# Optimization experiments

Measured on AMD Instinct MI355X. Metric: run time of the kernel, lower is better.

Reference implementation:

```python
import jax, jax.numpy as jnp
import numpy as np

B, S, HID = 2, 2048, 4096
H, HKV = 32, 8
D = HID // H  # 128
THETA = 10000.0


def rope(x, positions):
    # x: [B, S, h, D]; rotate-half RoPE
    half = D // 2
    inv_freq = 1.0 / (THETA ** (jnp.arange(0, half, dtype=jnp.float32) / half))
    ang = positions[:, None].astype(jnp.float32) * inv_freq[None, :]  # [S, half]
    cos = jnp.cos(ang)[None, :, None, :]
    sin = jnp.sin(ang)[None, :, None, :]
    x1, x2 = x[..., :half], x[..., half:]
    return jnp.concatenate([x1 * cos - x2 * sin, x2 * cos + x1 * sin], axis=-1)


def setup_inputs() -> dict:
    key = jax.random.key(0)
    k1, k2, k3, k4, k5 = jax.random.split(key, 5)
    sc = 1.0 / np.sqrt(HID)
    return {
        "x": jax.random.normal(k1, (B, S, HID), dtype=jnp.float32),
        "wq": jax.random.normal(k2, (HID, HID), dtype=jnp.float32) * sc,
        "wk": jax.random.normal(k3, (HID, HKV * D), dtype=jnp.float32) * sc,
        "wv": jax.random.normal(k4, (HID, HKV * D), dtype=jnp.float32) * sc,
        "wo": jax.random.normal(k5, (HID, HID), dtype=jnp.float32) * sc,
    }


def reference(x, wq, wk, wv, wo):
    pos = jnp.arange(S)
    q = (x @ wq).reshape(B, S, H, D)
    k = (x @ wk).reshape(B, S, HKV, D)
    v = (x @ wv).reshape(B, S, HKV, D)
    q = rope(q, pos)
    k = rope(k, pos)
    # GQA: repeat kv heads to match query heads
    rep = H // HKV
    k = jnp.repeat(k, rep, axis=2)  # [B, S, H, D]
    v = jnp.repeat(v, rep, axis=2)
    scale = 1.0 / jnp.sqrt(jnp.float32(D))
    scores = jnp.einsum('bqhd,bkhd->bhqk', q, k) * scale  # [B, H, S, S]
    causal = jnp.tril(jnp.ones((S, S), dtype=bool))
    scores = jnp.where(causal[None, None], scores, jnp.finfo(scores.dtype).min)
    attn = jax.nn.softmax(scores, axis=-1)
    out = jnp.einsum('bhqk,bkhd->bqhd', attn, v).reshape(B, S, HID)
    return out @ wo
```

## Files before the change

kernel.cpp:

```cpp
#include <hip/hip_runtime.h>

#define BATCH 2
#define SEQ   2048
#define HIDSZ 4096
#define NH    32
#define NKV   8
#define HD    128
#define HALFD 64
#define MROWS (BATCH*SEQ)
#define KVDIM (NKV*HD)

typedef _Float16 f16;
typedef __attribute__((ext_vector_type(4))) float    fx4;
typedef __attribute__((ext_vector_type(4))) _Float16 half4;
typedef __attribute__((ext_vector_type(8))) _Float16 half8;

__device__ __forceinline__ float ldf(const f16* p)   { return (float)*p; }
__device__ __forceinline__ float ldf(const float* p) { return *p; }
__device__ __forceinline__ void  stf(f16* p, float v)   { *p = (f16)v; }
__device__ __forceinline__ void  stf(float* p, float v) { *p = v; }

template<typename T> struct avec;
template<> struct avec<float> { using type = fx4; };
template<> struct avec<f16>   { using type = half4; };

__device__ __forceinline__ half4 toh4(fx4 v) {
    half4 h; h[0] = (f16)v[0]; h[1] = (f16)v[1]; h[2] = (f16)v[2]; h[3] = (f16)v[3];
    return h;
}
__device__ __forceinline__ half4 toh4(half4 v) { return v; }

template<typename TA, typename TC>
__global__ __launch_bounds__(256)
void gemm_mfma(const TA* __restrict__ A, const float* __restrict__ B,
               TC* __restrict__ C, int M, int N, int K) {
    __shared__ f16 As[128][32];
    __shared__ f16 Bs[128][32];
    const int tid  = threadIdx.x;
    const int wave = tid >> 6, lane = tid & 63;
    const int c    = lane & 15, qd = lane >> 4;
    const int wr   = (wave >> 1) * 64, wc = (wave & 1) * 64;
    const int bx = blockIdx.x, by = blockIdx.y;

    const int am = tid >> 3;
    const int ak = (tid & 7) * 4;
    const int bn = (tid & 31) * 4;
    const int bk = (tid >> 5) * 4;

    const TA*    Ap = A + (size_t)(by * 128 + am) * K + ak;
    const float* Bp = B + (size_t)bk * N + bx * 128 + bn;

    fx4 acc[4][4];
#pragma unroll
    for (int i = 0; i < 4; i++)
#pragma unroll
        for (int j = 0; j < 4; j++)
#pragma unroll
            for (int r = 0; r < 4; r++) acc[i][j][r] = 0.f;

    using AT = typename avec<TA>::type;
    AT  areg[4];
    fx4 breg[4];
#pragma unroll
    for (int u = 0; u < 4; u++) {
        areg[u] = *(const AT*)(Ap + (size_t)u * 32 * K);
        breg[u] = *(const fx4*)(Bp + (size_t)u * N);
    }

    for (int k0 = 0; k0 < K; k0 += 32) {
#pragma unroll
        for (int u = 0; u < 4; u++)
            *(half4*)&As[am + u * 32][ak] = toh4(areg[u]);
#pragma unroll
        for (int v = 0; v < 4; v++) {
            const int n  = bn + v;
            const int kx = bk ^ (8 * ((n >> 2) & 3));
            half4 h;
#pragma unroll
            for (int u = 0; u < 4; u++) h[u] = (f16)breg[u][v];
            *(half4*)&Bs[n][kx] = h;
        }
        __syncthreads();
        if (k0 + 32 < K) {
#pragma unroll
            for (int u = 0; u < 4; u++) {
                areg[u] = *(const AT*)(Ap + (size_t)u * 32 * K + (k0 + 32));
                breg[u] = *(const fx4*)(Bp + (size_t)(k0 + 32 + u) * N);
            }
        }
        half8 af[4], bf[4];
#pragma unroll
        for (int i = 0; i < 4; i++)
            af[i] = *(const half8*)&As[wr + i * 16 + c][qd * 8];
#pragma unroll
        for (int j = 0; j < 4; j++) {
            const int n = wc + j * 16 + c;
            bf[j] = *(const half8*)&Bs[n][(qd * 8) ^ (8 * ((n >> 2) & 3))];
        }
#pragma unroll
        for (int i = 0; i < 4; i++)
#pragma unroll
            for (int j = 0; j < 4; j++)
                acc[i][j] = __builtin_amdgcn_mfma_f32_16x16x32_f16(
                                af[i], bf[j], acc[i][j], 0, 0, 0);
        __syncthreads();
    }

#pragma unroll
    for (int i = 0; i < 4; i++)
#pragma unroll
        for (int j = 0; j < 4; j++)
#pragma unroll
            for (int r = 0; r < 4; r++)
                stf(&C[(size_t)(by * 128 + wr + i * 16 + qd * 4 + r) * N
                       + bx * 128 + wc + j * 16 + c], acc[i][j][r]);
}

template<typename T>
__global__ void rope_kernel(T* __restrict__ t, int heads) {
    int idx = blockIdx.x * blockDim.x + threadIdx.x;
    int i   = idx & (HALFD - 1);
    int r   = idx >> 6;
    int h   = r % heads;
    int row = r / heads;
    int pos = row & (SEQ - 1);
    float inv_freq = expf(-(float)i * (9.210340371976184f / 64.0f));
    float ang = (float)pos * inv_freq;
    float s, c;
    sincosf(ang, &s, &c);
    size_t base = (size_t)row * ((size_t)heads * HD) + (size_t)h * HD;
    float x1 = ldf(&t[base + i]);
    float x2 = ldf(&t[base + i + HALFD]);
    stf(&t[base + i],         x1 * c - x2 * s);
    stf(&t[base + i + HALFD], x2 * c + x1 * s);
}

__global__ __launch_bounds__(256)
void transpose_v_kernel(const f16* __restrict__ v, f16* __restrict__ vt) {
    __shared__ short tile[32][33];
    int ts = blockIdx.x * 32;
    int td = blockIdx.y * 32;
    int bk = blockIdx.z;
    int b = bk >> 3, kvh = bk & 7;
    int tx = threadIdx.x & 31, ty = threadIdx.x >> 5;
    const short* vp = (const short*)v;
    short* vtp = (short*)vt;
#pragma unroll
    for (int i = 0; i < 4; i++) {
        int s = ts + ty + i * 8;
        tile[ty + i * 8][tx] = vp[(size_t)(b * SEQ + s) * KVDIM + kvh * HD + td + tx];
    }
    __syncthreads();
#pragma unroll
    for (int i = 0; i < 4; i++) {
        int d = td + ty + i * 8;
        vtp[((size_t)(b * NKV + kvh) * HD + d) * SEQ + ts + tx] = tile[tx][ty + i * 8];
    }
}

__global__ __launch_bounds__(256)
void flash_attn_kernel(const f16* __restrict__ q, const f16* __restrict__ k,
                       const f16* __restrict__ vt, f16* __restrict__ ao) {
    const int NT = SEQ / 64;
    int h = blockIdx.y, b = blockIdx.z;
    int kvh = h >> 2;
    int tid = threadIdx.x;
    int wave = tid >> 6, lane = tid & 63;
    int col = lane & 15, quad = lane >> 4;

    __shared__ f16 Ks[64 * 128];
    __shared__ f16 Vs[128 * 64];
    __shared__ f16 Ps[4 * 16 * 64];

    const f16* kg0 = k  + (size_t)(b * SEQ) * KVDIM + kvh * HD;
    const f16* vg0 = vt + ((size_t)(b * NKV + kvh) * HD) * SEQ;
    const float scale = 0.08838834764831845f;

#pragma unroll 1
    for (int hf = 0; hf < 2; ++hf) {
        const int qv  = hf ? (NT - 1 - (int)blockIdx.x) : (int)blockIdx.x;
        const int q0  = qv * 64;
        const int nkv = qv + 1;

        half8 qf[4];
        {
            const f16* qbase = q +
                (size_t)(b * SEQ + q0 + wave * 16 + col) * HIDSZ + h * HD + quad * 8;
#pragma unroll
            for (int ks = 0; ks < 4; ks++)
                qf[ks] = *(const half8*)(qbase + ks * 32);
        }

        float m_i[4], l_i[4];
#pragma unroll
        for (int r = 0; r < 4; r++) { m_i[r] = -1e30f; l_i[r] = 0.f; }
        fx4 O[8];
#pragma unroll
        for (int n = 0; n < 8; n++)
#pragma unroll
            for (int r = 0; r < 4; r++) O[n][r] = 0.f;

        half8 kreg[4], vreg[4];
#pragma unroll
        for (int i = 0; i < 4; i++) {
            int c2 = tid + i * 256, row = c2 >> 4, d0 = (c2 & 15) * 8;
            kreg[i] = *(const half8*)(kg0 + (size_t)row * KVDIM + d0);
        }
#pragma unroll
        for (int i = 0; i < 4; i++) {
            int c2 = tid + i * 256, row = c2 >> 3, s0 = (c2 & 7) * 8;
            vreg[i] = *(const half8*)(vg0 + (size_t)row * SEQ + s0);
        }
        __syncthreads();
#pragma unroll
        for (int i = 0; i < 4; i++) {
            int c2 = tid + i * 256, row = c2 >> 4, d0 = (c2 & 15) * 8;
            *(half8*)&Ks[row * 128 + (d0 ^ ((row & 7) << 3))] = kreg[i];
        }
#pragma unroll
        for (int i = 0; i < 4; i++) {
            int c2 = tid + i * 256, row = c2 >> 3, s0 = (c2 & 7) * 8;
            *(half8*)&Vs[row * 64 + (s0 ^ ((row & 7) << 3))] = vreg[i];
        }
        __syncthreads();

#pragma unroll 1
        for (int t = 0; t < nkv; ++t) {
            const int j0  = t * 64;
            const bool pre = (t + 1 < nkv);
            if (pre) {
                const int jn = j0 + 64;
#pragma unroll
                for (int i = 0; i < 4; i++) {
                    int c2 = tid + i * 256, row = c2 >> 4, d0 = (c2 & 15) * 8;
                    kreg[i] = *(const half8*)(kg0 + (size_t)(jn + row) * KVDIM + d0);
                }
#pragma unroll
                for (int i = 0; i < 4; i++) {
                    int c2 = tid + i * 256, row = c2 >> 3, s0 = (c2 & 7) * 8;
                    vreg[i] = *(const half8*)(vg0 + (size_t)row * SEQ + jn + s0);
                }
            }
            fx4 S[4];
#pragma unroll
            for (int nt = 0; nt < 4; nt++) {
                fx4 acc;
#pragma unroll
                for (int r = 0; r < 4; r++) acc[r] = 0.f;
                const int row = nt * 16 + col;
#pragma unroll
                for (int ks = 0; ks < 4; ks++) {
                    half8 kf = *(const half8*)&Ks[row * 128 +
                                   ((ks * 32 + quad * 8) ^ ((row & 7) << 3))];
                    acc = __builtin_amdgcn_mfma_f32_16x16x32_f16(qf[ks], kf, acc, 0, 0, 0);
                }
#pragma unroll
                for (int r = 0; r < 4; r++) S[nt][r] = acc[r] * scale;
            }
            if (j0 == q0) {
                int rowb = wave * 16 + quad * 4;
#pragma unroll
                for (int nt = 0; nt < 4; nt++)
#pragma unroll
                    for (int r = 0; r < 4; r++)
                        if (nt * 16 + col > rowb + r) S[nt][r] = -1e30f;
            }
            float mn[4], alpha[4];
#pragma unroll
            for (int r = 0; r < 4; r++) {
                float mx = fmaxf(fmaxf(S[0][r], S[1][r]), fmaxf(S[2][r], S[3][r]));
#pragma unroll
                for (int d = 8; d >= 1; d >>= 1) mx = fmaxf(mx, __shfl_xor(mx, d, 64));
                mn[r] = fmaxf(m_i[r], mx);
                alpha[r] = __expf(m_i[r] - mn[r]);
                m_i[r] = mn[r];
            }
#pragma unroll
            for (int nt = 0; nt < 4; nt++)
#pragma unroll
                for (int r = 0; r < 4; r++) S[nt][r] = __expf(S[nt][r] - mn[r]);
#pragma unroll
            for (int r = 0; r < 4; r++) {
                float s = (S[0][r] + S[1][r]) + (S[2][r] + S[3][r]);
#pragma unroll
                for (int d = 8; d >= 1; d >>= 1) s += __shfl_xor(s, d, 64);
                l_i[r] = l_i[r] * alpha[r] + s;
            }
#pragma unroll
            for (int n = 0; n < 8; n++)
#pragma unroll
                for (int r = 0; r < 4; r++) O[n][r] *= alpha[r];
#pragma unroll
            for (int nt = 0; nt < 4; nt++)
#pragma unroll
                for (int r = 0; r < 4; r++) {
                    int prow = quad * 4 + r;
                    Ps[wave * 1024 + prow * 64 +
                       ((nt * 16 + col) ^ ((prow & 7) << 3))] = (f16)S[nt][r];
                }
            half8 pf[2];
#pragma unroll
            for (int ks2 = 0; ks2 < 2; ks2++)
                pf[ks2] = *(const half8*)&Ps[wave * 1024 + col * 64 +
                              ((ks2 * 32 + quad * 8) ^ ((col & 7) << 3))];
#pragma unroll
            for (int n = 0; n < 8; n++) {
                const int row = n * 16 + col;
#pragma unroll
                for (int ks2 = 0; ks2 < 2; ks2++) {
                    half8 vf = *(const half8*)&Vs[row * 64 +
                                   ((ks2 * 32 + quad * 8) ^ ((row & 7) << 3))];
                    O[n] = __builtin_amdgcn_mfma_f32_16x16x32_f16(pf[ks2], vf, O[n], 0, 0, 0);
                }
            }
            if (pre) {
                __syncthreads();
#pragma unroll
                for (int i = 0; i < 4; i++) {
                    int c2 = tid + i * 256, row = c2 >> 4, d0 = (c2 & 15) * 8;
                    *(half8*)&Ks[row * 128 + (d0 ^ ((row & 7) << 3))] = kreg[i];
                }
#pragma unroll
                for (int i = 0; i < 4; i++) {
                    int c2 = tid + i * 256, row = c2 >> 3, s0 = (c2 & 7) * 8;
                    *(half8*)&Vs[row * 64 + (s0 ^ ((row & 7) << 3))] = vreg[i];
                }
                __syncthreads();
            }
        }

#pragma unroll
        for (int r = 0; r < 4; r++) l_i[r] = 1.f / l_i[r];
        int orow = q0 + wave * 16 + quad * 4;
#pragma unroll
        for (int n = 0; n < 8; n++)
#pragma unroll
            for (int r = 0; r < 4; r++)
                ao[(size_t)(b * SEQ + orow + r) * HIDSZ + h * HD + n * 16 + col] =
                    (f16)(O[n][r] * l_i[r]);
    }
}

extern "C" void kernel_launch(void* const* d_in, const int* in_sizes, int n_in,
                              void* d_out, int out_size, void* d_ws, size_t ws_size,
                              hipStream_t stream) {
    const float* x  = (const float*)d_in[0];
    const float* wq = (const float*)d_in[1];
    const float* wk = (const float*)d_in[2];
    const float* wv = (const float*)d_in[3];
    const float* wo = (const float*)d_in[4];
    float* out = (float*)d_out;

    f16* q  = (f16*)d_ws;
    f16* k  = q + (size_t)MROWS * HIDSZ;
    f16* v  = k + (size_t)MROWS * KVDIM;
    f16* ao = v + (size_t)MROWS * KVDIM;
    f16* vt = ao + (size_t)MROWS * HIDSZ;

    gemm_mfma<float, f16><<<dim3(HIDSZ / 128, MROWS / 128), 256, 0, stream>>>(
        x, wq, q, MROWS, HIDSZ, HIDSZ);
    gemm_mfma<float, f16><<<dim3(KVDIM / 128, MROWS / 128), 256, 0, stream>>>(
        x, wk, k, MROWS, KVDIM, HIDSZ);
    gemm_mfma<float, f16><<<dim3(KVDIM / 128, MROWS / 128), 256, 0, stream>>>(
        x, wv, v, MROWS, KVDIM, HIDSZ);

    rope_kernel<f16><<<(MROWS * NH * HALFD) / 256, 256, 0, stream>>>(q, NH);
    rope_kernel<f16><<<(MROWS * NKV * HALFD) / 256, 256, 0, stream>>>(k, NKV);

    transpose_v_kernel<<<dim3(SEQ / 32, HD / 32, BATCH * NKV), 256, 0, stream>>>(v, vt);

    flash_attn_kernel<<<dim3(SEQ / 128, NH, BATCH), 256, 0, stream>>>(q, k, vt, ao);

    gemm_mfma<f16, float><<<dim3(HIDSZ / 128, MROWS / 128), 256, 0, stream>>>(
        ao, wo, out, MROWS, HIDSZ, HIDSZ);
}
```

Before: 1.159 ms.

## Pad GEMM LDS tiles, remap B loads to scalar columns, swizzle block order

Pads the As/Bs shared tiles from 32 to 40 halves per row, which replaces the XOR swizzle as the way to avoid LDS bank conflicts. The B tile load is remapped so each thread reads scalar floats along four k rows for strided columns, instead of float4 vectors along n, and writes one contiguous half4 per column. Workgroup IDs are remapped in groups of 8 to change the tile visiting order for L2 reuse. The cost is narrower global loads for B (four scalar loads instead of one vector load per row) and more LDS footprint.

```diff
diff --git a/kernel.cpp b/kernel.cpp
--- a/kernel.cpp
+++ b/kernel.cpp
@@ -34,21 +34,25 @@
 __global__ __launch_bounds__(256)
 void gemm_mfma(const TA* __restrict__ A, const float* __restrict__ B,
                TC* __restrict__ C, int M, int N, int K) {
-    __shared__ f16 As[128][32];
-    __shared__ f16 Bs[128][32];
+    __shared__ f16 As[128][40];
+    __shared__ f16 Bs[128][40];
     const int tid  = threadIdx.x;
     const int wave = tid >> 6, lane = tid & 63;
     const int c    = lane & 15, qd = lane >> 4;
     const int wr   = (wave >> 1) * 64, wc = (wave & 1) * 64;
-    const int bx = blockIdx.x, by = blockIdx.y;
+
+    const int nwg = gridDim.x * gridDim.y;
+    const int lin = blockIdx.y * gridDim.x + blockIdx.x;
+    const int swz = (lin & 7) * (nwg >> 3) + (lin >> 3);
+    const int bx  = swz % gridDim.x, by = swz / gridDim.x;
 
     const int am = tid >> 3;
     const int ak = (tid & 7) * 4;
-    const int bn = (tid & 31) * 4;
-    const int bk = (tid >> 5) * 4;
+    const int bc = tid & 31;
+    const int kb = (tid >> 5) * 4;
 
     const TA*    Ap = A + (size_t)(by * 128 + am) * K + ak;
-    const float* Bp = B + (size_t)bk * N + bx * 128 + bn;
+    const float* Bp = B + (size_t)kb * N + bx * 128 + bc;
 
     fx4 acc[4][4];
 #pragma unroll
@@ -59,12 +63,14 @@
             for (int r = 0; r < 4; r++) acc[i][j][r] = 0.f;
 
     using AT = typename avec<TA>::type;
-    AT  areg[4];
-    fx4 breg[4];
+    AT    areg[4];
+    float breg[4][4];
 #pragma unroll
     for (int u = 0; u < 4; u++) {
         areg[u] = *(const AT*)(Ap + (size_t)u * 32 * K);
-        breg[u] = *(const fx4*)(Bp + (size_t)u * N);
+#pragma unroll
+        for (int kk = 0; kk < 4; kk++)
+            breg[u][kk] = Bp[(size_t)kk * N + u * 32];
     }
 
     for (int k0 = 0; k0 < K; k0 += 32) {
@@ -72,20 +78,20 @@
         for (int u = 0; u < 4; u++)
             *(half4*)&As[am + u * 32][ak] = toh4(areg[u]);
 #pragma unroll
-        for (int v = 0; v < 4; v++) {
-            const int n  = bn + v;
-            const int kx = bk ^ (8 * ((n >> 2) & 3));
+        for (int u = 0; u < 4; u++) {
             half4 h;
 #pragma unroll
-            for (int u = 0; u < 4; u++) h[u] = (f16)breg[u][v];
-            *(half4*)&Bs[n][kx] = h;
+            for (int kk = 0; kk < 4; kk++) h[kk] = (f16)breg[u][kk];
+            *(half4*)&Bs[bc + u * 32][kb] = h;
         }
         __syncthreads();
         if (k0 + 32 < K) {
 #pragma unroll
             for (int u = 0; u < 4; u++) {
                 areg[u] = *(const AT*)(Ap + (size_t)u * 32 * K + (k0 + 32));
-                breg[u] = *(const fx4*)(Bp + (size_t)(k0 + 32 + u) * N);
+#pragma unroll
+                for (int kk = 0; kk < 4; kk++)
+                    breg[u][kk] = Bp[(size_t)(k0 + 32 + kk) * N + u * 32];
             }
         }
         half8 af[4], bf[4];
@@ -93,10 +99,8 @@
         for (int i = 0; i < 4; i++)
             af[i] = *(const half8*)&As[wr + i * 16 + c][qd * 8];
 #pragma unroll
-        for (int j = 0; j < 4; j++) {
-            const int n = wc + j * 16 + c;
-            bf[j] = *(const half8*)&Bs[n][(qd * 8) ^ (8 * ((n >> 2) & 3))];
-        }
+        for (int j = 0; j < 4; j++)
+            bf[j] = *(const half8*)&Bs[wc + j * 16 + c][qd * 8];
 #pragma unroll
         for (int i = 0; i < 4; i++)
 #pragma unroll
```

Result: no change. 1.175 ms (+1.4%).

## Pre-transpose weights to fp16 and stream B tiles via async global-to-LDS loads

Applied to the files above, without the earlier changes.

Each weight matrix is first transposed and converted to fp16 by a new kernel into workspace. The GEMMs then load B tiles straight into double-buffered LDS with global_load_lds, with an XOR swizzle, in place of the register-staged fp32 load and per-element conversion. This halves the B bytes each GEMM reads and frees registers and VALU work in the inner loop. The cost is four extra transpose kernels that read full fp32 weights each call, plus aliasing of workspace buffers (ao and woT reuse wT and q).

```diff
diff --git a/kernel.cpp b/kernel.cpp
--- a/kernel.cpp
+++ b/kernel.cpp
@@ -11,6 +11,7 @@
 #define KVDIM (NKV*HD)
 
 typedef _Float16 f16;
+typedef __attribute__((ext_vector_type(2))) _Float16 half2v;
 typedef __attribute__((ext_vector_type(4))) float    fx4;
 typedef __attribute__((ext_vector_type(4))) _Float16 half4;
 typedef __attribute__((ext_vector_type(8))) _Float16 half8;
@@ -20,6 +21,36 @@
 __device__ __forceinline__ void  stf(f16* p, float v)   { *p = (f16)v; }
 __device__ __forceinline__ void  stf(float* p, float v) { *p = v; }
 
+__device__ __forceinline__ void async_ld16(const void* g, void* l) {
+    __builtin_amdgcn_global_load_lds(
+        (const __attribute__((address_space(1))) void*)g,
+        (__attribute__((address_space(3))) void*)l,
+        16, 0, 0);
+}
+
+__global__ __launch_bounds__(256)
+void wtrans_kernel(const float* __restrict__ w, f16* __restrict__ wt,
+                   int K, int N) {
+    __shared__ float tile[32][33];
+    int tn = blockIdx.x * 32;
+    int tk = blockIdx.y * 32;
+    int tx = threadIdx.x & 31, ty = threadIdx.x >> 5;
+#pragma unroll
+    for (int i = 0; i < 4; i++)
+        tile[ty + i * 8][tx] = w[(size_t)(tk + ty + i * 8) * N + tn + tx];
+    __syncthreads();
+    int nl0 = threadIdx.x >> 4;
+    int kp  = (threadIdx.x & 15) * 2;
+#pragma unroll
+    for (int p = 0; p < 2; p++) {
+        int nl = p * 16 + nl0;
+        half2v h2;
+        h2[0] = (f16)tile[kp][nl];
+        h2[1] = (f16)tile[kp + 1][nl];
+        *(half2v*)&wt[(size_t)(tn + nl) * K + tk + kp] = h2;
+    }
+}
+
 template<typename T> struct avec;
 template<> struct avec<float> { using type = fx4; };
 template<> struct avec<f16>   { using type = half4; };
@@ -32,10 +63,10 @@
 
 template<typename TA, typename TC>
 __global__ __launch_bounds__(256)
-void gemm_mfma(const TA* __restrict__ A, const float* __restrict__ B,
-               TC* __restrict__ C, int M, int N, int K) {
-    __shared__ f16 As[128][32];
-    __shared__ f16 Bs[128][32];
+void gemm_bt(const TA* __restrict__ A, const f16* __restrict__ BT,
+             TC* __restrict__ C, int M, int N, int K) {
+    __shared__ f16 As[128][40];
+    __shared__ f16 Bs[2][128 * 32];
     const int tid  = threadIdx.x;
     const int wave = tid >> 6, lane = tid & 63;
     const int c    = lane & 15, qd = lane >> 4;
@@ -44,11 +75,13 @@
 
     const int am = tid >> 3;
     const int ak = (tid & 7) * 4;
-    const int bn = (tid & 31) * 4;
-    const int bk = (tid >> 5) * 4;
-
-    const TA*    Ap = A + (size_t)(by * 128 + am) * K + ak;
-    const float* Bp = B + (size_t)bk * N + bx * 128 + bn;
+    const TA* Ap = A + (size_t)(by * 128 + am) * K + ak;
+
+    const int bn = wave * 16 + (lane >> 2);
+    const int kc = (lane & 3) ^ ((bn >> 1) & 3);
+    const f16* Bp0 = BT + (size_t)(bx * 128 + bn) * K + kc * 8;
+    const f16* Bp1 = BT + (size_t)(bx * 128 + bn + 64) * K + kc * 8;
+    f16* ldsB0 = &Bs[0][wave * 512];
 
     fx4 acc[4][4];
 #pragma unroll
@@ -59,34 +92,28 @@
             for (int r = 0; r < 4; r++) acc[i][j][r] = 0.f;
 
     using AT = typename avec<TA>::type;
-    AT  areg[4];
-    fx4 breg[4];
-#pragma unroll
-    for (int u = 0; u < 4; u++) {
+    AT areg[4];
+#pragma unroll
+    for (int u = 0; u < 4; u++)
         areg[u] = *(const AT*)(Ap + (size_t)u * 32 * K);
-        breg[u] = *(const fx4*)(Bp + (size_t)u * N);
-    }
-
+
+    async_ld16(Bp0, ldsB0);
+    async_ld16(Bp1, ldsB0 + 2048);
+
+    int cur = 0;
     for (int k0 = 0; k0 < K; k0 += 32) {
 #pragma unroll
         for (int u = 0; u < 4; u++)
             *(half4*)&As[am + u * 32][ak] = toh4(areg[u]);
-#pragma unroll
-        for (int v = 0; v < 4; v++) {
-            const int n  = bn + v;
-            const int kx = bk ^ (8 * ((n >> 2) & 3));
-            half4 h;
-#pragma unroll
-            for (int u = 0; u < 4; u++) h[u] = (f16)breg[u][v];
-            *(half4*)&Bs[n][kx] = h;
-        }
         __syncthreads();
-        if (k0 + 32 < K) {
-#pragma unroll
-            for (int u = 0; u < 4; u++) {
+        const bool pre = (k0 + 32) < K;
+        if (pre) {
+#pragma unroll
+            for (int u = 0; u < 4; u++)
                 areg[u] = *(const AT*)(Ap + (size_t)u * 32 * K + (k0 + 32));
-                breg[u] = *(const fx4*)(Bp + (size_t)(k0 + 32 + u) * N);
-            }
+            f16* dst = &Bs[cur ^ 1][wave * 512];
+            async_ld16(Bp0 + (k0 + 32), dst);
+            async_ld16(Bp1 + (k0 + 32), dst + 2048);
         }
         half8 af[4], bf[4];
 #pragma unroll
@@ -95,7 +122,7 @@
 #pragma unroll
         for (int j = 0; j < 4; j++) {
             const int n = wc + j * 16 + c;
-            bf[j] = *(const half8*)&Bs[n][(qd * 8) ^ (8 * ((n >> 2) & 3))];
+            bf[j] = *(const half8*)&Bs[cur][n * 32 + ((qd ^ ((n >> 1) & 3)) * 8)];
         }
 #pragma unroll
         for (int i = 0; i < 4; i++)
@@ -104,6 +131,7 @@
                 acc[i][j] = __builtin_amdgcn_mfma_f32_16x16x32_f16(
                                 af[i], bf[j], acc[i][j], 0, 0, 0);
         __syncthreads();
+        cur ^= 1;
     }
 
 #pragma unroll
@@ -244,18 +272,18 @@
             fx4 S[4];
 #pragma unroll
             for (int nt = 0; nt < 4; nt++) {
-                fx4 acc;
-#pragma unroll
-                for (int r = 0; r < 4; r++) acc[r] = 0.f;
+                fx4 acc2;
+#pragma unroll
+                for (int r = 0; r < 4; r++) acc2[r] = 0.f;
                 const int row = nt * 16 + col;
 #pragma unroll
                 for (int ks = 0; ks < 4; ks++) {
                     half8 kf = *(const half8*)&Ks[row * 128 +
                                    ((ks * 32 + quad * 8) ^ ((row & 7) << 3))];
-                    acc = __builtin_amdgcn_mfma_f32_16x16x32_f16(qf[ks], kf, acc, 0, 0, 0);
-                }
-#pragma unroll
-                for (int r = 0; r < 4; r++) S[nt][r] = acc[r] * scale;
+                    acc2 = __builtin_amdgcn_mfma_f32_16x16x32_f16(qf[ks], kf, acc2, 0, 0, 0);
+                }
+#pragma unroll
+                for (int r = 0; r < 4; r++) S[nt][r] = acc2[r] * scale;
             }
             if (j0 == q0) {
                 int rowb = wave * 16 + quad * 4;
@@ -351,18 +379,25 @@
     const float* wo = (const float*)d_in[4];
     float* out = (float*)d_out;
 
-    f16* q  = (f16*)d_ws;
-    f16* k  = q + (size_t)MROWS * HIDSZ;
-    f16* v  = k + (size_t)MROWS * KVDIM;
-    f16* ao = v + (size_t)MROWS * KVDIM;
-    f16* vt = ao + (size_t)MROWS * HIDSZ;
-
-    gemm_mfma<float, f16><<<dim3(HIDSZ / 128, MROWS / 128), 256, 0, stream>>>(
-        x, wq, q, MROWS, HIDSZ, HIDSZ);
-    gemm_mfma<float, f16><<<dim3(KVDIM / 128, MROWS / 128), 256, 0, stream>>>(
-        x, wk, k, MROWS, KVDIM, HIDSZ);
-    gemm_mfma<float, f16><<<dim3(KVDIM / 128, MROWS / 128), 256, 0, stream>>>(
-        x, wv, v, MROWS, KVDIM, HIDSZ);
+    f16* wT = (f16*)d_ws;
+    f16* q  = wT + (size_t)HIDSZ * HIDSZ;
+    f16* k  = q  + (size_t)MROWS * HIDSZ;
+    f16* v  = k  + (size_t)MROWS * KVDIM;
+    f16* vt = v  + (size_t)MROWS * KVDIM;
+    f16* ao  = wT;
+    f16* woT = q;
+
+    wtrans_kernel<<<dim3(HIDSZ / 32, HIDSZ / 32), 256, 0, stream>>>(wq, wT, HIDSZ, HIDSZ);
+    gemm_bt<float, f16><<<dim3(HIDSZ / 128, MROWS / 128), 256, 0, stream>>>(
+        x, wT, q, MROWS, HIDSZ, HIDSZ);
+
+    wtrans_kernel<<<dim3(KVDIM / 32, HIDSZ / 32), 256, 0, stream>>>(wk, wT, HIDSZ, KVDIM);
+    gemm_bt<float, f16><<<dim3(KVDIM / 128, MROWS / 128), 256, 0, stream>>>(
+        x, wT, k, MROWS, KVDIM, HIDSZ);
+
+    wtrans_kernel<<<dim3(KVDIM / 32, HIDSZ / 32), 256, 0, stream>>>(wv, wT, HIDSZ, KVDIM);
+    gemm_bt<float, f16><<<dim3(KVDIM / 128, MROWS / 128), 256, 0, stream>>>(
+        x, wT, v, MROWS, KVDIM, HIDSZ);
 
     rope_kernel<f16><<<(MROWS * NH * HALFD) / 256, 256, 0, stream>>>(q, NH);
     rope_kernel<f16><<<(MROWS * NKV * HALFD) / 256, 256, 0, stream>>>(k, NKV);
@@ -371,6 +406,7 @@
 
     flash_attn_kernel<<<dim3(SEQ / 128, NH, BATCH), 256, 0, stream>>>(q, k, vt, ao);
 
-    gemm_mfma<f16, float><<<dim3(HIDSZ / 128, MROWS / 128), 256, 0, stream>>>(
-        ao, wo, out, MROWS, HIDSZ, HIDSZ);
-}
+    wtrans_kernel<<<dim3(HIDSZ / 32, HIDSZ / 32), 256, 0, stream>>>(wo, woT, HIDSZ, HIDSZ);
+    gemm_bt<f16, float><<<dim3(HIDSZ / 128, MROWS / 128), 256, 0, stream>>>(
+        ao, woT, out, MROWS, HIDSZ, HIDSZ);
+}
```

New measurement: 1.104 ms. 1.05x faster.
